# Optimization experiments

Hardware: AMD Instinct MI355X
Metric: run time of the kernel (lower is better)

## Reference

```python
import jax, jax.numpy as jnp
import numpy as np

NUM_HEADS = 16
NUM_BUCKETS = 32
MAX_DISTANCE = 128


def _relative_position_bucket(relative_position, num_buckets=NUM_BUCKETS, max_distance=MAX_DISTANCE):
    # bidirectional=True (encoder self-attention)
    nb = num_buckets // 2  # 16
    buckets = (relative_position > 0).astype(jnp.int32) * nb
    rp = jnp.abs(relative_position)
    max_exact = nb // 2  # 8
    is_small = rp < max_exact
    # log-spaced bins for large distances; clamp arg of log to >=1 to avoid log(0)
    rp_f = jnp.maximum(rp, 1).astype(jnp.float32)
    large = max_exact + (
        jnp.log(rp_f / max_exact) / np.log(max_distance / max_exact) * (nb - max_exact)
    ).astype(jnp.int32)
    large = jnp.minimum(large, nb - 1)
    return buckets + jnp.where(is_small, rp, large)


def setup_inputs() -> dict:
    key = jax.random.key(0)
    ks = jax.random.split(key, 6)
    B, L, D = 2, 2048, 1024
    scale = 0.02  # keep activations in a sane range
    return {
        "hidden_states": jax.random.normal(ks[0], (B, L, D), dtype=jnp.float32),
        "Wq": jax.random.normal(ks[1], (D, D), dtype=jnp.float32) * scale,
        "Wk": jax.random.normal(ks[2], (D, D), dtype=jnp.float32) * scale,
        "Wv": jax.random.normal(ks[3], (D, D), dtype=jnp.float32) * scale,
        "Wo": jax.random.normal(ks[4], (D, D), dtype=jnp.float32) * scale,
        "bias_table": jax.random.normal(ks[5], (NUM_BUCKETS, NUM_HEADS), dtype=jnp.float32),
    }


def reference(hidden_states, Wq, Wk, Wv, Wo, bias_table):
    B, L, D = hidden_states.shape
    H = NUM_HEADS
    hd = D // H

    # projections (nn.Linear: y = x @ W.T), split heads -> [B, H, L, hd]
    def proj(x, W):
        return (x @ W.T).reshape(B, L, H, hd).transpose(0, 2, 1, 3)

    q = proj(hidden_states, Wq)
    k = proj(hidden_states, Wk)
    v = proj(hidden_states, Wv)

    # T5 relative position bias: [1, H, L, L]
    ctx = jnp.arange(L)[:, None]
    mem = jnp.arange(L)[None, :]
    buckets = _relative_position_bucket(mem - ctx)  # [L, L]
    position_bias = bias_table[buckets].transpose(2, 0, 1)[None]  # [1, H, L, L]

    # NOTE: T5-style attention has NO 1/sqrt(hd) scaling
    scores = jnp.einsum("bhqd,bhkd->bhqk", q, k) + position_bias
    attn = jax.nn.softmax(scores.astype(jnp.float32), axis=-1).astype(scores.dtype)
    out = jnp.einsum("bhqk,bhkd->bhqd", attn, v)
    out = out.transpose(0, 2, 1, 3).reshape(B, L, D)
    out = out @ Wo.T
    return out, position_bias
```

## Files before the change

### kernel.cpp

```cpp
#include <hip/hip_runtime.h>
#include <cstdint>
#include <cmath>

typedef unsigned short ushort_t;
typedef __bf16 bf16x8 __attribute__((ext_vector_type(8)));
typedef float f32x4 __attribute__((ext_vector_type(4)));
typedef ushort_t us4 __attribute__((ext_vector_type(4)));
typedef ushort_t us8 __attribute__((ext_vector_type(8)));

#define MFMA16(a, b, c) __builtin_amdgcn_mfma_f32_16x16x32_bf16(a, b, c, 0, 0, 0)
#define LOG2E 1.4426950408889634f

__device__ __forceinline__ ushort_t f2bf(float f) {
    union { __bf16 h; ushort_t u; } cv;
    cv.h = (__bf16)f;
    return cv.u;
}

__device__ __forceinline__ void glds16(const ushort_t* g, ushort_t* s) {
    __builtin_amdgcn_global_load_lds(
        (const __attribute__((address_space(1))) void*)(g),
        (__attribute__((address_space(3))) void*)(s), 16, 0, 0);
}

__global__ void cast_all_k(const float* __restrict__ x, const float* __restrict__ wq,
                           const float* __restrict__ wk, const float* __restrict__ wv,
                           const float* __restrict__ wo, ushort_t* __restrict__ xb,
                           ushort_t* __restrict__ wb, unsigned char* __restrict__ lut) {
    int id = blockIdx.x, t = threadIdx.x;
    if (id == 8192) {
        for (int idx = t; idx < 4095; idx += 256) {
            int rel = idx - 2047;
            int bb = (rel > 0) ? 16 : 0;
            int rp = (rel < 0) ? -rel : rel;
            int add;
            if (rp < 8) {
                add = rp;
            } else {
                float lg = (float)::log((double)rp * 0.125);
                double tt = ((double)lg) / 2.772588722239781 * 8.0;
                int large = 8 + (int)tt;
                add = (large < 15) ? large : 15;
            }
            lut[idx] = (unsigned char)(bb + add);
        }
        return;
    }
    const float* src;
    ushort_t* dst;
    int idx;
    float scale = 1.0f;
    if (id < 4096) {
        src = x; dst = xb; idx = id * 256 + t;
    } else {
        int r = (id - 4096) >> 10;
        idx = ((id - 4096) & 1023) * 256 + t;
        src = (r == 0) ? wq : (r == 1) ? wk : (r == 2) ? wv : wo;
        dst = wb + (size_t)r * 1048576;
        if (r == 0) scale = LOG2E;
    }
    float4 v = ((const float4*)src)[idx];
    us4 o;
    o.x = f2bf(v.x * scale); o.y = f2bf(v.y * scale);
    o.z = f2bf(v.z * scale); o.w = f2bf(v.w * scale);
    ((us4*)dst)[idx] = o;
}

template <int MODE>
__global__ __launch_bounds__(256) void gemm_bt_k(const ushort_t* __restrict__ A,
                                                 const ushort_t* __restrict__ B0,
                                                 void* __restrict__ C0,
                                                 int M, int N, int K, long sB, long sC) {
    __shared__ ushort_t As[128 * 64];
    __shared__ ushort_t Bs[128 * 64];
    const int tid = threadIdx.x;
    const int l = tid & 63, w = tid >> 6;
    const int quad = l >> 4, lc = l & 15;
    const int wm = w >> 1, wn = w & 1;
    const int m0 = blockIdx.y * 128, n0 = blockIdx.x * 128;
    const ushort_t* B = B0 + (long)blockIdx.z * sB;

    f32x4 acc[4][4] = {};
    const int rA = l >> 3;
    const int cA = ((l & 7) ^ rA) * 8;

    for (int k0 = 0; k0 < K; k0 += 64) {
#pragma unroll
        for (int t = 0; t < 4; ++t) {
            int row = w * 32 + t * 8;
            glds16(A + (size_t)(m0 + row + rA) * K + k0 + cA, &As[row * 64]);
            glds16(B + (size_t)(n0 + row + rA) * K + k0 + cA, &Bs[row * 64]);
        }
        __syncthreads();
#pragma unroll
        for (int ko = 0; ko < 2; ++ko) {
            const int ch = (((ko * 4 + quad) ^ (lc & 7))) * 8;
            bf16x8 af[4], bfr[4];
#pragma unroll
            for (int mt = 0; mt < 4; ++mt)
                af[mt] = *(const bf16x8*)&As[(wm * 64 + mt * 16 + lc) * 64 + ch];
#pragma unroll
            for (int nt = 0; nt < 4; ++nt)
                bfr[nt] = *(const bf16x8*)&Bs[(wn * 64 + nt * 16 + lc) * 64 + ch];
#pragma unroll
            for (int mt = 0; mt < 4; ++mt)
#pragma unroll
                for (int nt = 0; nt < 4; ++nt)
                    acc[mt][nt] = MFMA16(af[mt], bfr[nt], acc[mt][nt]);
        }
        __syncthreads();
    }
#pragma unroll
    for (int mt = 0; mt < 4; ++mt) {
#pragma unroll
        for (int nt = 0; nt < 4; ++nt) {
            int col = n0 + wn * 64 + nt * 16 + lc;
#pragma unroll
            for (int r = 0; r < 4; ++r) {
                int row = m0 + wm * 64 + mt * 16 + quad * 4 + r;
                if constexpr (MODE == 1) {
                    ((float*)C0)[(size_t)row * N + col] = acc[mt][nt][r];
                } else if constexpr (MODE == 0) {
                    (((ushort_t*)C0) + (long)blockIdx.z * sC)[(size_t)row * N + col] = f2bf(acc[mt][nt][r]);
                } else {
                    ((ushort_t*)C0)[(size_t)(col >> 11) * 2097152 + (size_t)row * 2048 + (col & 2047)] =
                        f2bf(acc[mt][nt][r]);
                }
            }
        }
    }
}

__global__ __launch_bounds__(256) void gemm_qkvt_k(const ushort_t* __restrict__ Xb,
                                                   const ushort_t* __restrict__ Wb,
                                                   ushort_t* __restrict__ QKg,
                                                   ushort_t* __restrict__ VTg) {
    __shared__ ushort_t As[128 * 64];
    __shared__ ushort_t Bs[128 * 64];
    const int tid = threadIdx.x;
    const int l = tid & 63, w = tid >> 6;
    const int quad = l >> 4, lc = l & 15;
    const int wm = w >> 1, wn = w & 1;
    const int id = blockIdx.x;

    const ushort_t* A;
    const ushort_t* B;
    int m0, n0, z = 0;
    bool vt;
    if (id < 512) {
        vt = false; z = id >> 8;
        int r = id & 255;
        m0 = (r >> 3) * 128; n0 = (r & 7) * 128;
        A = Xb; B = Wb + z * 1048576;
    } else {
        vt = true;
        int r = id - 512;
        m0 = (r >> 5) * 128; n0 = (r & 31) * 128;
        A = Wb + 2097152; B = Xb;
    }

    f32x4 acc[4][4] = {};
    const int rA = l >> 3;
    const int cA = ((l & 7) ^ rA) * 8;

    for (int k0 = 0; k0 < 1024; k0 += 64) {
#pragma unroll
        for (int t = 0; t < 4; ++t) {
            int row = w * 32 + t * 8;
            glds16(A + (size_t)(m0 + row + rA) * 1024 + k0 + cA, &As[row * 64]);
            glds16(B + (size_t)(n0 + row + rA) * 1024 + k0 + cA, &Bs[row * 64]);
        }
        __syncthreads();
#pragma unroll
        for (int ko = 0; ko < 2; ++ko) {
            const int ch = (((ko * 4 + quad) ^ (lc & 7))) * 8;
            bf16x8 af[4], bfr[4];
#pragma unroll
            for (int mt = 0; mt < 4; ++mt)
                af[mt] = *(const bf16x8*)&As[(wm * 64 + mt * 16 + lc) * 64 + ch];
#pragma unroll
            for (int nt = 0; nt < 4; ++nt)
                bfr[nt] = *(const bf16x8*)&Bs[(wn * 64 + nt * 16 + lc) * 64 + ch];
#pragma unroll
            for (int mt = 0; mt < 4; ++mt)
#pragma unroll
                for (int nt = 0; nt < 4; ++nt)
                    acc[mt][nt] = MFMA16(af[mt], bfr[nt], acc[mt][nt]);
        }
        __syncthreads();
    }
#pragma unroll
    for (int mt = 0; mt < 4; ++mt) {
#pragma unroll
        for (int nt = 0; nt < 4; ++nt) {
            int col = n0 + wn * 64 + nt * 16 + lc;
#pragma unroll
            for (int r = 0; r < 4; ++r) {
                int row = m0 + wm * 64 + mt * 16 + quad * 4 + r;
                if (!vt) {
                    QKg[(size_t)z * 4194304 + (size_t)row * 1024 + col] = f2bf(acc[mt][nt][r]);
                } else {
                    VTg[(size_t)(col >> 11) * 2097152 + (size_t)row * 2048 + (col & 2047)] =
                        f2bf(acc[mt][nt][r]);
                }
            }
        }
    }
}

__global__ __launch_bounds__(256, 2) void attn_k(const ushort_t* __restrict__ Qg,
                                                 const ushort_t* __restrict__ Kg,
                                                 const ushort_t* __restrict__ VTg,
                                                 ushort_t* __restrict__ Ctx,
                                                 const unsigned char* __restrict__ lut,
                                                 const float* __restrict__ table,
                                                 float* __restrict__ bias_out) {
    __shared__ ushort_t Kbuf[2][128 * 64];
    __shared__ ushort_t Pws[4 * 32 * 40];
    __shared__ alignas(16) float diag4[2][4 * 256];

    const int tid = threadIdx.x, l = tid & 63, w = tid >> 6;
    const int quad = l >> 4, lc = l & 15;
    const int id = blockIdx.x;
    const int bh = id & 31, b = bh >> 4, h = bh & 15;
    const int q0 = (id >> 5) * 128;
    const size_t tokbase = (size_t)b * 2048;

    const int rK = l >> 3;
    const int cK = ((l & 7) ^ rK) * 8;

#pragma unroll
    for (int t = 0; t < 4; ++t) {
        int row0 = w * 32 + t * 8;
        glds16(Qg + (tokbase + q0 + row0 + rK) * 1024 + h * 64 + cK, &Kbuf[1][row0 * 64]);
        glds16(Kg + (tokbase + row0 + rK) * 1024 + h * 64 + cK, &Kbuf[0][row0 * 64]);
    }
    if (tid < 255) {
        float v0 = table[(int)lut[tid + 1920 - q0] * 16 + h];
        float* dg = diag4[0];
        dg[tid] = v0;
        if (tid >= 1) dg[255 + tid] = v0;
        if (tid >= 2) dg[510 + tid] = v0;
        if (tid >= 3) dg[765 + tid] = v0;
    }
    __syncthreads();

    bf16x8 qf[2][2];
#pragma unroll
    for (int nt = 0; nt < 2; ++nt)
#pragma unroll
        for (int ko = 0; ko < 2; ++ko) {
            int row = w * 32 + nt * 16 + lc;
            int ch = ((ko * 4 + quad) ^ (lc & 7)) * 8;
            qf[nt][ko] = *(const bf16x8*)&Kbuf[1][row * 64 + ch];
        }
    __syncthreads();

    float mstate[2] = {-1e30f, -1e30f};
    float lstate[2] = {0.f, 0.f};
    f32x4 acco[4][2] = {};
    ushort_t* Pw = &Pws[w * 1280];
    const int cb0 = quad * 4 - (w * 32 + lc) + 127;
    const int cxor = lc & 3;
    const ushort_t* VTbase = VTg + (size_t)(b * 1024 + h * 64) * 2048;

    const int bjf = (tid & 15) * 4 + b * 64;
    const int big = tid >> 4;
    const int d00 = bjf - big + 127;
    const int sb = cb0 & 3, bb = cb0 & ~3;
    const int ss = d00 & 3, db = d00 & ~3;

    for (int kt = 0; kt < 16; ++kt) {
        const int j0 = kt * 128;
        const int cur = kt & 1, nxt = cur ^ 1;
        const ushort_t* Kc = Kbuf[cur];
        const float* dc = diag4[cur];

        if (kt < 15) {
            const int jn = j0 + 128;
#pragma unroll
            for (int t = 0; t < 4; ++t) {
                int row0 = w * 32 + t * 8;
                glds16(Kg + (tokbase + jn + row0 + rK) * 1024 + h * 64 + cK, &Kbuf[nxt][row0 * 64]);
            }
            if (tid < 255) {
                float vv = table[(int)lut[jn - q0 + tid + 1920] * 16 + h];
                float* dg = diag4[nxt];
                dg[tid] = vv;
                if (tid >= 1) dg[255 + tid] = vv;
                if (tid >= 2) dg[510 + tid] = vv;
                if (tid >= 3) dg[765 + tid] = vv;
            }
        }

        bf16x8 vf[4][4];
#pragma unroll
        for (int kk = 0; kk < 4; ++kk)
#pragma unroll
            for (int dt = 0; dt < 4; ++dt)
                vf[kk][dt] = *(const bf16x8*)(VTbase + (size_t)(dt * 16 + lc) * 2048 +
                                              j0 + kk * 32 + quad * 8);

        {
            float* outp = bias_out + ((size_t)h * 2048 + q0) * 2048 + j0;
            const float* dsp = dc + ss * 256;
#pragma unroll
            for (int rr = 0; rr < 8; ++rr) {
                int il = big + 16 * rr;
                f32x4 v = *(const f32x4*)&dsp[db - 16 * rr];
                __builtin_nontemporal_store(v, (f32x4*)(outp + (size_t)il * 2048 + bjf));
            }
        }

        f32x4 accs[8][2] = {};
#pragma unroll
        for (int ko = 0; ko < 2; ++ko) {
            const int ch = ((ko * 4 + quad) ^ (lc & 7)) * 8;
#pragma unroll
            for (int mt = 0; mt < 8; ++mt) {
                bf16x8 kf = *(const bf16x8*)&Kc[(mt * 16 + lc) * 64 + ch];
                accs[mt][0] = MFMA16(kf, qf[0][ko], accs[mt][0]);
                accs[mt][1] = MFMA16(kf, qf[1][ko], accs[mt][1]);
            }
        }

        {
            const float* dcp = dc + sb * 256;
            f32x4 dprev4 = *(const f32x4*)&dcp[bb - 16];
#pragma unroll
            for (int mt = 0; mt < 8; ++mt) {
                f32x4 dcur4 = *(const f32x4*)&dcp[bb + mt * 16];
#pragma unroll
                for (int r = 0; r < 4; ++r) {
                    accs[mt][0][r] = fmaf(dcur4[r], LOG2E, accs[mt][0][r]);
                    accs[mt][1][r] = fmaf(dprev4[r], LOG2E, accs[mt][1][r]);
                }
                dprev4 = dcur4;
            }
        }

#pragma unroll
        for (int nt = 0; nt < 2; ++nt) {
            float mx = accs[0][nt][0];
#pragma unroll
            for (int mt = 0; mt < 8; ++mt)
#pragma unroll
                for (int r = 0; r < 4; ++r) mx = fmaxf(mx, accs[mt][nt][r]);
            mx = fmaxf(mx, __shfl_xor(mx, 16, 64));
            mx = fmaxf(mx, __shfl_xor(mx, 32, 64));
            float mo = mstate[nt], mn = fmaxf(mo, mx);
            float alpha = __builtin_amdgcn_exp2f(mo - mn);
            mstate[nt] = mn;
            float rs = 0.f;
#pragma unroll
            for (int mt = 0; mt < 8; ++mt)
#pragma unroll
                for (int r = 0; r < 4; ++r) {
                    float p = __builtin_amdgcn_exp2f(accs[mt][nt][r] - mn);
                    accs[mt][nt][r] = p;
                    rs += p;
                }
            rs += __shfl_xor(rs, 16, 64);
            rs += __shfl_xor(rs, 32, 64);
            lstate[nt] = lstate[nt] * alpha + rs;
#pragma unroll
            for (int dt = 0; dt < 4; ++dt) acco[dt][nt] *= alpha;
        }

#pragma unroll
        for (int kk = 0; kk < 4; ++kk) {
#pragma unroll
            for (int half = 0; half < 2; ++half) {
                int mt = kk * 2 + half;
                int c = half * 2 + (quad >> 1);
                int coff = ((c ^ cxor) * 8 + (quad & 1) * 4);
#pragma unroll
                for (int nt = 0; nt < 2; ++nt) {
                    us4 o;
#pragma unroll
                    for (int r = 0; r < 4; ++r) o[r] = f2bf(accs[mt][nt][r]);
                    *(us4*)&Pw[(nt * 16 + lc) * 40 + coff] = o;
                }
            }
            bf16x8 pf[2];
#pragma unroll
            for (int nt = 0; nt < 2; ++nt)
                pf[nt] = *(const bf16x8*)&Pw[(nt * 16 + lc) * 40 + (quad ^ cxor) * 8];
#pragma unroll
            for (int dt = 0; dt < 4; ++dt)
#pragma unroll
                for (int nt = 0; nt < 2; ++nt)
                    acco[dt][nt] = MFMA16(vf[kk][dt], pf[nt], acco[dt][nt]);
        }
        if (kt < 15) __syncthreads();
    }

#pragma unroll
    for (int nt = 0; nt < 2; ++nt) {
        float inv = 1.0f / lstate[nt];
        size_t row = tokbase + q0 + w * 32 + nt * 16 + lc;
#pragma unroll
        for (int dt = 0; dt < 4; ++dt) {
            us4 o;
#pragma unroll
            for (int r = 0; r < 4; ++r) o[r] = f2bf(acco[dt][nt][r] * inv);
            *(us4*)&Ctx[row * 1024 + h * 64 + dt * 16 + quad * 4] = o;
        }
    }
}

extern "C" void kernel_launch(void* const* d_in, const int* in_sizes, int n_in,
                              void* d_out, int out_size, void* d_ws, size_t ws_size,
                              hipStream_t stream) {
    const float* hidden = (const float*)d_in[0];
    const float* Wq = (const float*)d_in[1];
    const float* Wk = (const float*)d_in[2];
    const float* Wv = (const float*)d_in[3];
    const float* Wo = (const float*)d_in[4];
    const float* table = (const float*)d_in[5];

    char* ws = (char*)d_ws;
    ushort_t* Xb  = (ushort_t*)(ws);
    ushort_t* Wb  = (ushort_t*)(ws + 8388608);
    ushort_t* Qg  = (ushort_t*)(ws + 16777216);
    ushort_t* Kgp = (ushort_t*)(ws + 25165824);
    ushort_t* VTg = (ushort_t*)(ws + 33554432);
    ushort_t* Ctx = (ushort_t*)(ws + 41943040);
    unsigned char* lutp = (unsigned char*)(ws + 50331648);

    float* out0 = (float*)d_out;
    float* out1 = out0 + 4194304;

    cast_all_k<<<8193, 256, 0, stream>>>(hidden, Wq, Wk, Wv, Wo, Xb, Wb, lutp);

    gemm_qkvt_k<<<768, 256, 0, stream>>>(Xb, Wb, Qg, VTg);

    attn_k<<<dim3(512), 256, 0, stream>>>(Qg, Kgp, VTg, Ctx, lutp, table, out1);
    gemm_bt_k<1><<<dim3(8, 32, 1), 256, 0, stream>>>(Ctx, Wb + 3145728, (void*)out0,
                                                     4096, 1024, 1024, 0, 0);
}
```

Baseline: 417.4 us.

## Move position-bias output writes from attention kernel into QKV GEMM launch

The 256 MB position_bias tensor was previously written from inside the attention kernel's main loop. This moves that work into 256 extra blocks of the QKV projection GEMM launch. Each extra block builds a diagonal strip from the lookup table in shared memory and streams 128 rows with nontemporal stores. The aim is to overlap the memory-bound bias write with the compute-bound GEMM and to free bandwidth and instructions in the attention loop. The risk is that the bias blocks are scheduled first and contend for HBM bandwidth with GEMM tiles, and that their unaligned scalar LDS reads are slower.

```diff
diff --git a/kernel.cpp b/kernel.cpp
--- a/kernel.cpp
+++ b/kernel.cpp
@@ -134,27 +134,50 @@
 __global__ __launch_bounds__(256) void gemm_qkvt_k(const ushort_t* __restrict__ Xb,
                                                    const ushort_t* __restrict__ Wb,
                                                    ushort_t* __restrict__ QKg,
-                                                   ushort_t* __restrict__ VTg) {
+                                                   ushort_t* __restrict__ VTg,
+                                                   const unsigned char* __restrict__ lut,
+                                                   const float* __restrict__ table,
+                                                   float* __restrict__ bias_out) {
     __shared__ ushort_t As[128 * 64];
     __shared__ ushort_t Bs[128 * 64];
     const int tid = threadIdx.x;
+    const int id = blockIdx.x;
+
+    if (id < 256) {
+        const int h = id >> 4, q0 = (id & 15) * 128;
+        float* dgb = (float*)As;
+        for (int i = tid; i < 2175; i += 256)
+            dgb[i] = table[(int)lut[i + 1920 - q0] * 16 + h];
+        __syncthreads();
+        float* outp = bias_out + ((size_t)h * 2048 + q0) * 2048 + tid * 8;
+        for (int rr = 0; rr < 128; ++rr) {
+            const float* src = dgb + tid * 8 + 127 - rr;
+            f32x4 v0, v1;
+            v0[0] = src[0]; v0[1] = src[1]; v0[2] = src[2]; v0[3] = src[3];
+            v1[0] = src[4]; v1[1] = src[5]; v1[2] = src[6]; v1[3] = src[7];
+            float* op = outp + (size_t)rr * 2048;
+            __builtin_nontemporal_store(v0, (f32x4*)op);
+            __builtin_nontemporal_store(v1, (f32x4*)(op + 4));
+        }
+        return;
+    }
+
     const int l = tid & 63, w = tid >> 6;
     const int quad = l >> 4, lc = l & 15;
     const int wm = w >> 1, wn = w & 1;
-    const int id = blockIdx.x;
 
     const ushort_t* A;
     const ushort_t* B;
     int m0, n0, z = 0;
     bool vt;
-    if (id < 512) {
-        vt = false; z = id >> 8;
-        int r = id & 255;
+    if (id < 768) {
+        vt = false; z = (id - 256) >> 8;
+        int r = (id - 256) & 255;
         m0 = (r >> 3) * 128; n0 = (r & 7) * 128;
         A = Xb; B = Wb + z * 1048576;
     } else {
         vt = true;
-        int r = id - 512;
+        int r = id - 768;
         m0 = (r >> 5) * 128; n0 = (r & 31) * 128;
         A = Wb + 2097152; B = Xb;
     }
@@ -213,8 +236,7 @@
                                                  const ushort_t* __restrict__ VTg,
                                                  ushort_t* __restrict__ Ctx,
                                                  const unsigned char* __restrict__ lut,
-                                                 const float* __restrict__ table,
-                                                 float* __restrict__ bias_out) {
+                                                 const float* __restrict__ table) {
     __shared__ ushort_t Kbuf[2][128 * 64];
     __shared__ ushort_t Pws[4 * 32 * 40];
     __shared__ alignas(16) float diag4[2][4 * 256];
@@ -264,11 +286,7 @@
     const int cxor = lc & 3;
     const ushort_t* VTbase = VTg + (size_t)(b * 1024 + h * 64) * 2048;
 
-    const int bjf = (tid & 15) * 4 + b * 64;
-    const int big = tid >> 4;
-    const int d00 = bjf - big + 127;
     const int sb = cb0 & 3, bb = cb0 & ~3;
-    const int ss = d00 & 3, db = d00 & ~3;
 
     for (int kt = 0; kt < 16; ++kt) {
         const int j0 = kt * 128;
@@ -300,17 +318,6 @@
             for (int dt = 0; dt < 4; ++dt)
                 vf[kk][dt] = *(const bf16x8*)(VTbase + (size_t)(dt * 16 + lc) * 2048 +
                                               j0 + kk * 32 + quad * 8);
-
-        {
-            float* outp = bias_out + ((size_t)h * 2048 + q0) * 2048 + j0;
-            const float* dsp = dc + ss * 256;
-#pragma unroll
-            for (int rr = 0; rr < 8; ++rr) {
-                int il = big + 16 * rr;
-                f32x4 v = *(const f32x4*)&dsp[db - 16 * rr];
-                __builtin_nontemporal_store(v, (f32x4*)(outp + (size_t)il * 2048 + bjf));
-            }
-        }
 
         f32x4 accs[8][2] = {};
 #pragma unroll
@@ -433,9 +440,9 @@
 
     cast_all_k<<<8193, 256, 0, stream>>>(hidden, Wq, Wk, Wv, Wo, Xb, Wb, lutp);
 
-    gemm_qkvt_k<<<768, 256, 0, stream>>>(Xb, Wb, Qg, VTg);
-
-    attn_k<<<dim3(512), 256, 0, stream>>>(Qg, Kgp, VTg, Ctx, lutp, table, out1);
+    gemm_qkvt_k<<<1024, 256, 0, stream>>>(Xb, Wb, Qg, VTg, lutp, table, out1);
+
+    attn_k<<<dim3(512), 256, 0, stream>>>(Qg, Kgp, VTg, Ctx, lutp, table);
     gemm_bt_k<1><<<dim3(8, 32, 1), 256, 0, stream>>>(Ctx, Wb + 3145728, (void*)out0,
                                                      4096, 1024, 1024, 0, 0);
 }
```

Result: slower. 525.3 us (+25.8%).
